# Kernel tuning notes

Measured on AMD Instinct MI355X. Metric: run time of the kernel, lower is better.

## Reference

```python
import jax, jax.numpy as jnp
import numpy as np

DIM = 512
CTX = 768
GROUPS = 32
EPS = 1e-5


def setup_inputs() -> dict:
    key = jax.random.key(0)
    ks = jax.random.split(key, 12)
    B, H, W, S = 16, 64, 64, 256
    x = jax.random.normal(ks[0], (B, DIM, H, W), dtype=jnp.float32)
    context = jax.random.normal(ks[1], (B, S, CTX), dtype=jnp.float32)
    gn_w = jnp.ones((DIM,), jnp.float32)
    gn_b = jnp.zeros((DIM,), jnp.float32)
    ln_w = jnp.ones((CTX,), jnp.float32)
    ln_b = jnp.zeros((CTX,), jnp.float32)
    wq = jax.random.normal(ks[2], (DIM, DIM), jnp.float32) * (DIM ** -0.5)
    bq = jnp.zeros((DIM,), jnp.float32)
    wkv = jax.random.normal(ks[3], (2 * DIM, CTX), jnp.float32) * (CTX ** -0.5)
    bkv = jnp.zeros((2 * DIM,), jnp.float32)
    wo = jax.random.normal(ks[4], (DIM, DIM), jnp.float32) * (DIM ** -0.5)
    bo = jnp.zeros((DIM,), jnp.float32)
    return {"x": x, "context": context, "gn_w": gn_w, "gn_b": gn_b,
            "ln_w": ln_w, "ln_b": ln_b, "wq": wq, "bq": bq,
            "wkv": wkv, "bkv": bkv, "wo": wo, "bo": bo}


def reference(x, context, gn_w, gn_b, ln_w, ln_b, wq, bq, wkv, bkv, wo, bo):
    b, c, h, w = x.shape
    scale = c ** -0.5
    # GroupNorm over (channels-per-group, H, W)
    xr = x.reshape(b, GROUPS, -1)
    mu = xr.mean(-1, keepdims=True)
    var = xr.var(-1, keepdims=True)
    xn = ((xr - mu) * jax.lax.rsqrt(var + EPS)).reshape(b, c, h, w)
    xn = xn * gn_w[None, :, None, None] + gn_b[None, :, None, None]
    # 1x1 conv query projection as channel GEMM
    q = jnp.einsum('bchw,oc->bohw', xn, wq) + bq[None, :, None, None]
    q = q.reshape(b, c, h * w).transpose(0, 2, 1)  # b, hw, c
    # LayerNorm on context
    cm = context.mean(-1, keepdims=True)
    cv = context.var(-1, keepdims=True)
    cn = (context - cm) * jax.lax.rsqrt(cv + EPS) * ln_w + ln_b
    kv = cn @ wkv.T + bkv  # b, s, 2c
    k, v = jnp.split(kv, 2, axis=-1)
    sim = jnp.einsum('bic,bjc->bij', q, k) * scale
    attn = jax.nn.softmax(sim, axis=-1)
    out = jnp.einsum('bij,bjc->bic', attn, v)
    out = out.transpose(0, 2, 1).reshape(b, c, h, w)
    out = jnp.einsum('bchw,oc->bohw', out, wo) + bo[None, :, None, None]
    return out + x
```

## Files before the change

### kernel.cpp

```cpp
#include <hip/hip_runtime.h>

typedef unsigned short u16;
typedef __attribute__((ext_vector_type(8))) short short8;
typedef __attribute__((ext_vector_type(4))) float f32x4;

#define DIM 512
#define CTX 768
#define HW 4096
#define NB 16
#define NS 256
#define EPSV 1e-5f

__device__ inline u16 f2bf(float f) {
    union { float f; unsigned u; } x; x.f = f;
    unsigned r = x.u + 0x7fffu + ((x.u >> 16) & 1u);
    return (u16)(r >> 16);
}
__device__ inline float bf2f(u16 v) {
    union { unsigned u; float f; } x; x.u = (unsigned)v << 16; return x.f;
}

__global__ void gn_stats(const float* __restrict__ x, const float* __restrict__ gn_w,
                         const float* __restrict__ gn_b, float* __restrict__ ga,
                         float* __restrict__ gd) {
    const int bg = blockIdx.x;
    const int b = bg >> 5, g = bg & 31;
    const float* base = x + ((long)b * DIM + g * 16) * HW;
    float s1 = 0.f, s2 = 0.f;
    const int tid = threadIdx.x;
    for (int i = tid; i < 16384; i += 256) {
        float4 v = ((const float4*)base)[i];
        s1 += v.x + v.y + v.z + v.w;
        s2 += v.x * v.x + v.y * v.y + v.z * v.z + v.w * v.w;
    }
    __shared__ float r1[256], r2[256];
    r1[tid] = s1; r2[tid] = s2; __syncthreads();
    for (int s = 128; s > 0; s >>= 1) {
        if (tid < s) { r1[tid] += r1[tid + s]; r2[tid] += r2[tid + s]; }
        __syncthreads();
    }
    __shared__ float mu_s, rs_s;
    if (tid == 0) {
        float mu = r1[0] * (1.f / 65536.f);
        float var = r2[0] * (1.f / 65536.f) - mu * mu;
        mu_s = mu; rs_s = rsqrtf(var + EPSV);
    }
    __syncthreads();
    if (tid < 16) {
        int c = g * 16 + tid;
        float aa = rs_s * gn_w[c];
        ga[b * DIM + c] = aa;
        gd[b * DIM + c] = gn_b[c] - mu_s * aa;
    }
}

__global__ void gn_apply_t(const float* __restrict__ x, const float* __restrict__ ga,
                           const float* __restrict__ gd, u16* __restrict__ xnt) {
    const int b = blockIdx.y;
    const int c0 = (blockIdx.x & 7) * 64;
    const int p0 = (blockIdx.x >> 3) * 64;
    __shared__ u16 t[64][68];
    const int tid = threadIdx.x;
    const int tc = tid >> 4;
    const int tp = (tid & 15) * 4;
    #pragma unroll
    for (int i = 0; i < 4; i++) {
        const int c = c0 + tc + i * 16;
        const float a = ga[b * DIM + c];
        const float d = gd[b * DIM + c];
        float4 v = *(const float4*)&x[((long)b * DIM + c) * HW + p0 + tp];
        u16* dst = &t[tc + i * 16][tp];
        dst[0] = f2bf(v.x * a + d);
        dst[1] = f2bf(v.y * a + d);
        dst[2] = f2bf(v.z * a + d);
        dst[3] = f2bf(v.w * a + d);
    }
    __syncthreads();
    const int wp = tid >> 3;
    const int wc = (tid & 7) * 8;
    #pragma unroll
    for (int i = 0; i < 2; i++) {
        const int p = wp + i * 32;
        short8 o;
        #pragma unroll
        for (int k = 0; k < 8; k++) o[k] = t[wc + k][p];
        *(short8*)&xnt[((long)b * HW + p0 + p) * DIM + c0 + wc] = o;
    }
}

__global__ void ln_ctx(const float* __restrict__ ctx, const float* __restrict__ ln_w,
                       const float* __restrict__ ln_b, u16* __restrict__ cn) {
    const int row = blockIdx.x;
    const int tid = threadIdx.x;
    const float* r = ctx + (long)row * CTX;
    float v[3]; float s1 = 0.f, s2 = 0.f;
    #pragma unroll
    for (int i = 0; i < 3; i++) { v[i] = r[tid + i * 256]; s1 += v[i]; s2 += v[i] * v[i]; }
    __shared__ float r1[256], r2[256];
    r1[tid] = s1; r2[tid] = s2; __syncthreads();
    for (int s = 128; s > 0; s >>= 1) {
        if (tid < s) { r1[tid] += r1[tid + s]; r2[tid] += r2[tid + s]; }
        __syncthreads();
    }
    __shared__ float mu_s, rs_s;
    if (tid == 0) {
        float mu = r1[0] * (1.f / 768.f);
        float var = r2[0] * (1.f / 768.f) - mu * mu;
        mu_s = mu; rs_s = rsqrtf(var + EPSV);
    }
    __syncthreads();
    #pragma unroll
    for (int i = 0; i < 3; i++) {
        int idx = tid + i * 256;
        cn[(long)row * CTX + idx] = f2bf((v[i] - mu_s) * rs_s * ln_w[idx] + ln_b[idx]);
    }
}

__global__ void cvt_weights(const float* __restrict__ wq, const float* __restrict__ wkv,
                            const float* __restrict__ wo, u16* __restrict__ wqtb,
                            u16* __restrict__ wkvb, u16* __restrict__ wob) {
    int i = blockIdx.x * 256 + threadIdx.x;
    if (i < 262144) {
        wqtb[(i & 511) * 512 + (i >> 9)] = f2bf(wq[i]);
        wob[i] = f2bf(wo[i]);
    }
    if (i < 786432) wkvb[i] = f2bf(wkv[i]);
}

__global__ void kbias_k(const u16* __restrict__ k, const float* __restrict__ bq,
                        float* __restrict__ kbias) {
    const int row = blockIdx.x;
    const int tid = threadIdx.x;
    const u16* r = k + (long)row * DIM;
    float s = bf2f(r[tid]) * bq[tid] + bf2f(r[tid + 256]) * bq[tid + 256];
    __shared__ float red[256];
    red[tid] = s; __syncthreads();
    for (int st = 128; st > 0; st >>= 1) {
        if (tid < st) red[tid] += red[tid + st];
        __syncthreads();
    }
    if (tid == 0) kbias[row] = red[0];
}

template <int EPI>
__launch_bounds__(256, 2)
__global__ void gemm_nt(const u16* __restrict__ A, const u16* __restrict__ Bm,
                        const float* __restrict__ bias,
                        void* __restrict__ out0, void* __restrict__ out1,
                        int M, int N, int K, long batchA, long batchB,
                        long obatch, int ldo) {
    __shared__ u16 As[128][56];
    __shared__ u16 Bs[128][56];
    const int tid = threadIdx.x;
    const int lane = tid & 63;
    const int wave = tid >> 6;
    const int bb = blockIdx.y;
    const int tiles_n = N >> 7;
    const int m0 = (blockIdx.x / tiles_n) << 7;
    const int n0 = (blockIdx.x % tiles_n) << 7;
    const u16* Ab = A + (long)bb * batchA + (long)m0 * K;
    const u16* Bb = Bm + (long)bb * batchB + (long)n0 * K;

    const int sr = tid >> 2;
    const int sc = (tid & 3) << 3;
    const int l16 = lane & 15;
    const int quad = lane >> 4;
    const int wr = (wave >> 1) << 6;
    const int wc = (wave & 1) << 6;

    f32x4 acc[4][4] = {};

    for (int k0 = 0; k0 < K; k0 += 32) {
        __syncthreads();
        *(short8*)&As[sr][sc]      = *(const short8*)(Ab + (long)sr * K + k0 + sc);
        *(short8*)&As[sr + 64][sc] = *(const short8*)(Ab + (long)(sr + 64) * K + k0 + sc);
        *(short8*)&Bs[sr][sc]      = *(const short8*)(Bb + (long)sr * K + k0 + sc);
        *(short8*)&Bs[sr + 64][sc] = *(const short8*)(Bb + (long)(sr + 64) * K + k0 + sc);
        __syncthreads();
        short8 af[4], bfr[4];
        #pragma unroll
        for (int i = 0; i < 4; i++) af[i] = *(const short8*)&As[wr + i * 16 + l16][quad * 8];
        #pragma unroll
        for (int j = 0; j < 4; j++) bfr[j] = *(const short8*)&Bs[wc + j * 16 + l16][quad * 8];
        #pragma unroll
        for (int i = 0; i < 4; i++)
            #pragma unroll
            for (int j = 0; j < 4; j++)
                acc[i][j] = __builtin_amdgcn_mfma_f32_16x16x32_bf16(af[i], bfr[j], acc[i][j], 0, 0, 0);
    }

    #pragma unroll
    for (int i = 0; i < 4; i++) {
        #pragma unroll
        for (int r = 0; r < 4; r++) {
            const int row = m0 + wr + i * 16 + quad * 4 + r;
            #pragma unroll
            for (int j = 0; j < 4; j++) {
                const int col = n0 + wc + j * 16 + l16;
                float v = acc[i][j][r];
                if (EPI == 0) {
                    v += bias[col];
                    if (col < DIM) ((u16*)out0)[(long)bb * obatch + (long)row * ldo + col] = f2bf(v);
                    else           ((u16*)out1)[(long)bb * obatch + (long)row * ldo + (col - DIM)] = f2bf(v);
                } else if (EPI == 3) {
                    ((u16*)out0)[(long)bb * obatch + (long)row * ldo + col] = f2bf(v);
                } else {
                    ((u16*)out0)[(long)bb * obatch + (long)col * ldo + row] = f2bf(v);
                }
            }
        }
    }
}

__launch_bounds__(512, 4)
__global__ void flash_attn(const u16* __restrict__ xnt, const u16* __restrict__ Kq,
                           const u16* __restrict__ Vot, const float* __restrict__ kbias,
                           const float* __restrict__ bo, const float* __restrict__ x,
                           float* __restrict__ out) {
    __shared__ __align__(16) char fsm[78080];
    u16 (*As)[56]      = (u16(*)[56])(fsm);
    u16 (*Bs)[56]      = (u16(*)[56])(fsm + 14336);
    u16 (*P)[264]      = (u16(*)[264])(fsm);
    float (*red)[4]    = (float(*)[4])(fsm + 67584);
    float (*lbuf)[132] = (float(*)[132])(fsm + 69632);

    const int tid = threadIdx.x;
    const int lane = tid & 63;
    const int wave = tid >> 6;
    const int mw = wave >> 2;
    const int nw = wave & 3;
    const int l16 = lane & 15;
    const int quad = lane >> 4;
    const int b = blockIdx.y;
    const int m0 = blockIdx.x << 7;

    const u16* Ab = xnt + ((long)b * HW + m0) * DIM;
    const u16* Bb = Kq + (long)b * NS * DIM;

    f32x4 acc[4][4] = {};
    for (int k0 = 0; k0 < DIM; k0 += 32) {
        __syncthreads();
        {
            const int r = tid >> 2, c = (tid & 3) << 3;
            *(short8*)&As[r][c] = *(const short8*)(Ab + (long)r * DIM + k0 + c);
            const int r2 = tid >> 1, c2 = (tid & 1) << 4;
            *(short8*)&Bs[r2][c2]     = *(const short8*)(Bb + (long)r2 * DIM + k0 + c2);
            *(short8*)&Bs[r2][c2 + 8] = *(const short8*)(Bb + (long)r2 * DIM + k0 + c2 + 8);
        }
        __syncthreads();
        short8 af[4], bfr[4];
        #pragma unroll
        for (int i = 0; i < 4; i++) af[i] = *(const short8*)&As[mw * 64 + i * 16 + l16][quad * 8];
        #pragma unroll
        for (int j = 0; j < 4; j++) bfr[j] = *(const short8*)&Bs[nw * 64 + j * 16 + l16][quad * 8];
        #pragma unroll
        for (int i = 0; i < 4; i++)
            #pragma unroll
            for (int j = 0; j < 4; j++)
                acc[i][j] = __builtin_amdgcn_mfma_f32_16x16x32_bf16(af[i], bfr[j], acc[i][j], 0, 0, 0);
    }

    const float scale = 0.044194173824159216f;
    float kb[4];
    #pragma unroll
    for (int j = 0; j < 4; j++) kb[j] = kbias[b * NS + nw * 64 + j * 16 + l16];

    #pragma unroll
    for (int i = 0; i < 4; i++) {
        #pragma unroll
        for (int r = 0; r < 4; r++) {
            float m = -1e30f;
            #pragma unroll
            for (int j = 0; j < 4; j++) {
                float v = (acc[i][j][r] + kb[j]) * scale;
                acc[i][j][r] = v;
                m = fmaxf(m, v);
            }
            #pragma unroll
            for (int off = 1; off < 16; off <<= 1) m = fmaxf(m, __shfl_xor(m, off));
            if (l16 == 0) red[mw * 64 + i * 16 + quad * 4 + r][nw] = m;
        }
    }
    __syncthreads();
    float rsum[4][4];
    #pragma unroll
    for (int i = 0; i < 4; i++) {
        #pragma unroll
        for (int r = 0; r < 4; r++) {
            const int row = mw * 64 + i * 16 + quad * 4 + r;
            float4 rv = *(const float4*)red[row];
            float gm = fmaxf(fmaxf(rv.x, rv.y), fmaxf(rv.z, rv.w));
            float s = 0.f;
            #pragma unroll
            for (int j = 0; j < 4; j++) {
                float e = __expf(acc[i][j][r] - gm);
                acc[i][j][r] = e;
                s += e;
            }
            #pragma unroll
            for (int off = 1; off < 16; off <<= 1) s += __shfl_xor(s, off);
            rsum[i][r] = s;
        }
    }
    __syncthreads();
    #pragma unroll
    for (int i = 0; i < 4; i++)
        #pragma unroll
        for (int r = 0; r < 4; r++)
            if (l16 == 0) red[mw * 64 + i * 16 + quad * 4 + r][nw] = rsum[i][r];
    __syncthreads();
    #pragma unroll
    for (int i = 0; i < 4; i++) {
        #pragma unroll
        for (int r = 0; r < 4; r++) {
            const int row = mw * 64 + i * 16 + quad * 4 + r;
            float4 sv = *(const float4*)red[row];
            float inv = 1.f / (sv.x + sv.y + sv.z + sv.w);
            #pragma unroll
            for (int j = 0; j < 4; j++)
                P[row][nw * 64 + j * 16 + l16] = f2bf(acc[i][j][r] * inv);
        }
    }
    __syncthreads();

    const u16* Vb = Vot + ((long)b * DIM + nw * 32 + l16) * NS + quad * 8;
    for (int nc = 0; nc < 4; nc++) {
        f32x4 oacc[4][2];
        #pragma unroll
        for (int i = 0; i < 4; i++)
            #pragma unroll
            for (int jj = 0; jj < 2; jj++)
                oacc[i][jj] = (f32x4){0.f, 0.f, 0.f, 0.f};
        #pragma unroll
        for (int kk = 0; kk < 8; kk++) {
            short8 pf[4], vf[2];
            #pragma unroll
            for (int i = 0; i < 4; i++)
                pf[i] = *(const short8*)&P[mw * 64 + i * 16 + l16][kk * 32 + quad * 8];
            #pragma unroll
            for (int jj = 0; jj < 2; jj++)
                vf[jj] = *(const short8*)(Vb + (long)(nc * 128 + jj * 16) * NS + kk * 32);
            #pragma unroll
            for (int i = 0; i < 4; i++)
                #pragma unroll
                for (int jj = 0; jj < 2; jj++)
                    oacc[i][jj] = __builtin_amdgcn_mfma_f32_16x16x32_bf16(pf[i], vf[jj], oacc[i][jj], 0, 0, 0);
        }
        #pragma unroll
        for (int t = 0; t < 8; t++) {
            __syncthreads();
            if (nw == (t >> 1)) {
                const int jj = t & 1;
                #pragma unroll
                for (int i = 0; i < 4; i++)
                    #pragma unroll
                    for (int r = 0; r < 4; r++)
                        lbuf[l16][mw * 64 + i * 16 + quad * 4 + r] = oacc[i][jj][r];
            }
            __syncthreads();
            {
                const int cl = tid >> 5;
                const int p4 = (tid & 31) * 4;
                const int cg = nc * 128 + t * 16 + cl;
                const long idx = ((long)b * DIM + cg) * HW + m0 + p4;
                const float bv = bo[cg];
                float4 v0 = *(const float4*)&lbuf[cl][p4];
                float4 x0 = *(const float4*)&x[idx];
                v0.x += x0.x + bv; v0.y += x0.y + bv; v0.z += x0.z + bv; v0.w += x0.w + bv;
                *(float4*)&out[idx] = v0;
            }
        }
    }
}

extern "C" void kernel_launch(void* const* d_in, const int* in_sizes, int n_in,
                              void* d_out, int out_size, void* d_ws, size_t ws_size,
                              hipStream_t stream) {
    const float* x    = (const float*)d_in[0];
    const float* ctx  = (const float*)d_in[1];
    const float* gn_w = (const float*)d_in[2];
    const float* gn_b = (const float*)d_in[3];
    const float* ln_w = (const float*)d_in[4];
    const float* ln_b = (const float*)d_in[5];
    const float* wq   = (const float*)d_in[6];
    const float* bq   = (const float*)d_in[7];
    const float* wkv  = (const float*)d_in[8];
    const float* bkv  = (const float*)d_in[9];
    const float* wo   = (const float*)d_in[10];
    const float* bo   = (const float*)d_in[11];

    char* ws = (char*)d_ws;
    u16*   xnt  = (u16*)(ws + 0);
    u16*   cn   = (u16*)(ws + 67108864);
    u16*   kb_  = (u16*)(ws + 73400320);
    u16*   vb_  = (u16*)(ws + 77594624);
    u16*   Kq   = (u16*)(ws + 81788928);
    u16*   Vot  = (u16*)(ws + 85983232);
    u16*   wqtb = (u16*)(ws + 90177536);
    u16*   wkvb = (u16*)(ws + 90701824);
    u16*   wob  = (u16*)(ws + 92274688);
    float* ga   = (float*)(ws + 92798976);
    float* gd   = ga + NB * DIM;
    float* kbias = (float*)(ws + 92864512);

    gn_stats<<<dim3(NB * 32), dim3(256), 0, stream>>>(x, gn_w, gn_b, ga, gd);
    gn_apply_t<<<dim3(512, NB), dim3(256), 0, stream>>>(x, ga, gd, xnt);
    ln_ctx<<<dim3(NB * NS), dim3(256), 0, stream>>>(ctx, ln_w, ln_b, cn);
    cvt_weights<<<dim3(3072), dim3(256), 0, stream>>>(wq, wkv, wo, wqtb, wkvb, wob);

    gemm_nt<0><<<dim3(2 * 8, NB), dim3(256), 0, stream>>>(
        cn, wkvb, bkv, kb_, vb_, NS, 2 * DIM, CTX,
        (long)NS * CTX, 0, (long)NS * DIM, DIM);
    gemm_nt<3><<<dim3(2 * 4, NB), dim3(256), 0, stream>>>(
        kb_, wqtb, nullptr, Kq, nullptr, NS, DIM, DIM,
        (long)NS * DIM, 0, (long)NS * DIM, DIM);
    kbias_k<<<dim3(NB * NS), dim3(256), 0, stream>>>(kb_, bq, kbias);
    gemm_nt<5><<<dim3(2 * 4, NB), dim3(256), 0, stream>>>(
        vb_, wob, nullptr, Vot, nullptr, NS, DIM, DIM,
        (long)NS * DIM, 0, (long)DIM * NS, NS);
    flash_attn<<<dim3(32, NB), dim3(512), 0, stream>>>(
        xnt, Kq, Vot, kbias, bo, x, (float*)d_out);
}
```

Before: 441.9 us.

## Register-prefetch GEMM tiles, merge Q/V projection launches, write attention output directly

In the GEMMs and the flash attention QK loop, the next K-slice is loaded into registers while MFMAs run on the current shared-memory tile, which overlaps global-load latency with compute. The two small projection GEMMs (K·Wq and V·Wo) are merged into one launch using blockIdx.z, removing a launch and filling more CUs. The attention epilogue no longer stages through shared memory with 16 barriers; each lane writes float4 results plus bias and residual straight to global memory. The cost is higher register pressure and possibly less coalesced stores in the epilogue.

```diff
diff --git a/kernel.cpp b/kernel.cpp
--- a/kernel.cpp
+++ b/kernel.cpp
@@ -142,24 +142,20 @@
     if (tid == 0) kbias[row] = red[0];
 }
 
-template <int EPI>
 __launch_bounds__(256, 2)
-__global__ void gemm_nt(const u16* __restrict__ A, const u16* __restrict__ Bm,
+__global__ void gemm_kv(const u16* __restrict__ A, const u16* __restrict__ Bm,
                         const float* __restrict__ bias,
-                        void* __restrict__ out0, void* __restrict__ out1,
-                        int M, int N, int K, long batchA, long batchB,
-                        long obatch, int ldo) {
+                        u16* __restrict__ outk, u16* __restrict__ outv) {
     __shared__ u16 As[128][56];
     __shared__ u16 Bs[128][56];
     const int tid = threadIdx.x;
     const int lane = tid & 63;
     const int wave = tid >> 6;
     const int bb = blockIdx.y;
-    const int tiles_n = N >> 7;
-    const int m0 = (blockIdx.x / tiles_n) << 7;
-    const int n0 = (blockIdx.x % tiles_n) << 7;
-    const u16* Ab = A + (long)bb * batchA + (long)m0 * K;
-    const u16* Bb = Bm + (long)bb * batchB + (long)n0 * K;
+    const int m0 = (blockIdx.x >> 3) << 7;
+    const int n0 = (blockIdx.x & 7) << 7;
+    const u16* Ab = A + (long)bb * NS * CTX + (long)m0 * CTX;
+    const u16* Bb = Bm + (long)n0 * CTX;
 
     const int sr = tid >> 2;
     const int sc = (tid & 3) << 3;
@@ -168,15 +164,29 @@
     const int wr = (wave >> 1) << 6;
     const int wc = (wave & 1) << 6;
 
+    const u16* Ap0 = Ab + (long)sr * CTX + sc;
+    const u16* Ap1 = Ab + (long)(sr + 64) * CTX + sc;
+    const u16* Bp0 = Bb + (long)sr * CTX + sc;
+    const u16* Bp1 = Bb + (long)(sr + 64) * CTX + sc;
+    short8 rA0 = *(const short8*)Ap0;
+    short8 rA1 = *(const short8*)Ap1;
+    short8 rB0 = *(const short8*)Bp0;
+    short8 rB1 = *(const short8*)Bp1;
+
     f32x4 acc[4][4] = {};
-
-    for (int k0 = 0; k0 < K; k0 += 32) {
-        __syncthreads();
-        *(short8*)&As[sr][sc]      = *(const short8*)(Ab + (long)sr * K + k0 + sc);
-        *(short8*)&As[sr + 64][sc] = *(const short8*)(Ab + (long)(sr + 64) * K + k0 + sc);
-        *(short8*)&Bs[sr][sc]      = *(const short8*)(Bb + (long)sr * K + k0 + sc);
-        *(short8*)&Bs[sr + 64][sc] = *(const short8*)(Bb + (long)(sr + 64) * K + k0 + sc);
-        __syncthreads();
+    for (int k0 = 0; k0 < CTX; k0 += 32) {
+        if (k0) __syncthreads();
+        *(short8*)&As[sr][sc]      = rA0;
+        *(short8*)&As[sr + 64][sc] = rA1;
+        *(short8*)&Bs[sr][sc]      = rB0;
+        *(short8*)&Bs[sr + 64][sc] = rB1;
+        __syncthreads();
+        if (k0 + 32 < CTX) {
+            rA0 = *(const short8*)(Ap0 + k0 + 32);
+            rA1 = *(const short8*)(Ap1 + k0 + 32);
+            rB0 = *(const short8*)(Bp0 + k0 + 32);
+            rB1 = *(const short8*)(Bp1 + k0 + 32);
+        }
         short8 af[4], bfr[4];
         #pragma unroll
         for (int i = 0; i < 4; i++) af[i] = *(const short8*)&As[wr + i * 16 + l16][quad * 8];
@@ -197,16 +207,83 @@
             #pragma unroll
             for (int j = 0; j < 4; j++) {
                 const int col = n0 + wc + j * 16 + l16;
-                float v = acc[i][j][r];
-                if (EPI == 0) {
-                    v += bias[col];
-                    if (col < DIM) ((u16*)out0)[(long)bb * obatch + (long)row * ldo + col] = f2bf(v);
-                    else           ((u16*)out1)[(long)bb * obatch + (long)row * ldo + (col - DIM)] = f2bf(v);
-                } else if (EPI == 3) {
-                    ((u16*)out0)[(long)bb * obatch + (long)row * ldo + col] = f2bf(v);
-                } else {
-                    ((u16*)out0)[(long)bb * obatch + (long)col * ldo + row] = f2bf(v);
-                }
+                float v = acc[i][j][r] + bias[col];
+                if (col < DIM) outk[(long)bb * NS * DIM + (long)row * DIM + col] = f2bf(v);
+                else           outv[(long)bb * NS * DIM + (long)row * DIM + (col - DIM)] = f2bf(v);
+            }
+        }
+    }
+}
+
+__launch_bounds__(256, 2)
+__global__ void gemm_qv(const u16* __restrict__ kb_, const u16* __restrict__ vb_,
+                        const u16* __restrict__ wqtb, const u16* __restrict__ wob,
+                        u16* __restrict__ Kq, u16* __restrict__ Vot) {
+    __shared__ u16 As[128][56];
+    __shared__ u16 Bs[128][56];
+    const int tid = threadIdx.x;
+    const int lane = tid & 63;
+    const int wave = tid >> 6;
+    const int bb = blockIdx.y;
+    const bool isV = blockIdx.z != 0;
+    const int m0 = (blockIdx.x >> 2) << 7;
+    const int n0 = (blockIdx.x & 3) << 7;
+    const u16* Ab = (isV ? vb_ : kb_) + (long)bb * NS * DIM + (long)m0 * DIM;
+    const u16* Bb = (isV ? wob : wqtb) + (long)n0 * DIM;
+
+    const int sr = tid >> 2;
+    const int sc = (tid & 3) << 3;
+    const int l16 = lane & 15;
+    const int quad = lane >> 4;
+    const int wr = (wave >> 1) << 6;
+    const int wc = (wave & 1) << 6;
+
+    const u16* Ap0 = Ab + (long)sr * DIM + sc;
+    const u16* Ap1 = Ab + (long)(sr + 64) * DIM + sc;
+    const u16* Bp0 = Bb + (long)sr * DIM + sc;
+    const u16* Bp1 = Bb + (long)(sr + 64) * DIM + sc;
+    short8 rA0 = *(const short8*)Ap0;
+    short8 rA1 = *(const short8*)Ap1;
+    short8 rB0 = *(const short8*)Bp0;
+    short8 rB1 = *(const short8*)Bp1;
+
+    f32x4 acc[4][4] = {};
+    for (int k0 = 0; k0 < DIM; k0 += 32) {
+        if (k0) __syncthreads();
+        *(short8*)&As[sr][sc]      = rA0;
+        *(short8*)&As[sr + 64][sc] = rA1;
+        *(short8*)&Bs[sr][sc]      = rB0;
+        *(short8*)&Bs[sr + 64][sc] = rB1;
+        __syncthreads();
+        if (k0 + 32 < DIM) {
+            rA0 = *(const short8*)(Ap0 + k0 + 32);
+            rA1 = *(const short8*)(Ap1 + k0 + 32);
+            rB0 = *(const short8*)(Bp0 + k0 + 32);
+            rB1 = *(const short8*)(Bp1 + k0 + 32);
+        }
+        short8 af[4], bfr[4];
+        #pragma unroll
+        for (int i = 0; i < 4; i++) af[i] = *(const short8*)&As[wr + i * 16 + l16][quad * 8];
+        #pragma unroll
+        for (int j = 0; j < 4; j++) bfr[j] = *(const short8*)&Bs[wc + j * 16 + l16][quad * 8];
+        #pragma unroll
+        for (int i = 0; i < 4; i++)
+            #pragma unroll
+            for (int j = 0; j < 4; j++)
+                acc[i][j] = __builtin_amdgcn_mfma_f32_16x16x32_bf16(af[i], bfr[j], acc[i][j], 0, 0, 0);
+    }
+
+    #pragma unroll
+    for (int i = 0; i < 4; i++) {
+        #pragma unroll
+        for (int r = 0; r < 4; r++) {
+            const int row = m0 + wr + i * 16 + quad * 4 + r;
+            #pragma unroll
+            for (int j = 0; j < 4; j++) {
+                const int col = n0 + wc + j * 16 + l16;
+                const u16 v = f2bf(acc[i][j][r]);
+                if (!isV) Kq[(long)bb * NS * DIM + (long)row * DIM + col] = v;
+                else      Vot[(long)bb * DIM * NS + (long)col * NS + row] = v;
             }
         }
     }
@@ -217,12 +294,11 @@
                            const u16* __restrict__ Vot, const float* __restrict__ kbias,
                            const float* __restrict__ bo, const float* __restrict__ x,
                            float* __restrict__ out) {
-    __shared__ __align__(16) char fsm[78080];
+    __shared__ __align__(16) char fsm[69632];
     u16 (*As)[56]      = (u16(*)[56])(fsm);
     u16 (*Bs)[56]      = (u16(*)[56])(fsm + 14336);
     u16 (*P)[264]      = (u16(*)[264])(fsm);
     float (*red)[4]    = (float(*)[4])(fsm + 67584);
-    float (*lbuf)[132] = (float(*)[132])(fsm + 69632);
 
     const int tid = threadIdx.x;
     const int lane = tid & 63;
@@ -237,17 +313,26 @@
     const u16* Ab = xnt + ((long)b * HW + m0) * DIM;
     const u16* Bb = Kq + (long)b * NS * DIM;
 
+    const int rS = tid >> 2, cS = (tid & 3) << 3;
+    const int rB = tid >> 1, cB = (tid & 1) << 4;
+    const u16* Ap = Ab + (long)rS * DIM + cS;
+    const u16* Bp = Bb + (long)rB * DIM + cB;
+    short8 rA  = *(const short8*)(Ap);
+    short8 rB0 = *(const short8*)(Bp);
+    short8 rB1 = *(const short8*)(Bp + 8);
+
     f32x4 acc[4][4] = {};
     for (int k0 = 0; k0 < DIM; k0 += 32) {
-        __syncthreads();
-        {
-            const int r = tid >> 2, c = (tid & 3) << 3;
-            *(short8*)&As[r][c] = *(const short8*)(Ab + (long)r * DIM + k0 + c);
-            const int r2 = tid >> 1, c2 = (tid & 1) << 4;
-            *(short8*)&Bs[r2][c2]     = *(const short8*)(Bb + (long)r2 * DIM + k0 + c2);
-            *(short8*)&Bs[r2][c2 + 8] = *(const short8*)(Bb + (long)r2 * DIM + k0 + c2 + 8);
-        }
-        __syncthreads();
+        if (k0) __syncthreads();
+        *(short8*)&As[rS][cS]     = rA;
+        *(short8*)&Bs[rB][cB]     = rB0;
+        *(short8*)&Bs[rB][cB + 8] = rB1;
+        __syncthreads();
+        if (k0 + 32 < DIM) {
+            rA  = *(const short8*)(Ap + k0 + 32);
+            rB0 = *(const short8*)(Bp + k0 + 32);
+            rB1 = *(const short8*)(Bp + k0 + 40);
+        }
         short8 af[4], bfr[4];
         #pragma unroll
         for (int i = 0; i < 4; i++) af[i] = *(const short8*)&As[mw * 64 + i * 16 + l16][quad * 8];
@@ -347,27 +432,19 @@
                     oacc[i][jj] = __builtin_amdgcn_mfma_f32_16x16x32_bf16(pf[i], vf[jj], oacc[i][jj], 0, 0, 0);
         }
         #pragma unroll
-        for (int t = 0; t < 8; t++) {
-            __syncthreads();
-            if (nw == (t >> 1)) {
-                const int jj = t & 1;
-                #pragma unroll
-                for (int i = 0; i < 4; i++)
-                    #pragma unroll
-                    for (int r = 0; r < 4; r++)
-                        lbuf[l16][mw * 64 + i * 16 + quad * 4 + r] = oacc[i][jj][r];
-            }
-            __syncthreads();
-            {
-                const int cl = tid >> 5;
-                const int p4 = (tid & 31) * 4;
-                const int cg = nc * 128 + t * 16 + cl;
-                const long idx = ((long)b * DIM + cg) * HW + m0 + p4;
-                const float bv = bo[cg];
-                float4 v0 = *(const float4*)&lbuf[cl][p4];
-                float4 x0 = *(const float4*)&x[idx];
-                v0.x += x0.x + bv; v0.y += x0.y + bv; v0.z += x0.z + bv; v0.w += x0.w + bv;
-                *(float4*)&out[idx] = v0;
+        for (int jj = 0; jj < 2; jj++) {
+            const int c = nc * 128 + nw * 32 + jj * 16 + l16;
+            const float bv = bo[c];
+            const long base = ((long)b * DIM + c) * HW + m0 + mw * 64 + quad * 4;
+            #pragma unroll
+            for (int i = 0; i < 4; i++) {
+                float4 xv = *(const float4*)&x[base + i * 16];
+                float4 o;
+                o.x = oacc[i][jj][0] + xv.x + bv;
+                o.y = oacc[i][jj][1] + xv.y + bv;
+                o.z = oacc[i][jj][2] + xv.z + bv;
+                o.w = oacc[i][jj][3] + xv.w + bv;
+                *(float4*)&out[base + i * 16] = o;
             }
         }
     }
@@ -408,16 +485,9 @@
     ln_ctx<<<dim3(NB * NS), dim3(256), 0, stream>>>(ctx, ln_w, ln_b, cn);
     cvt_weights<<<dim3(3072), dim3(256), 0, stream>>>(wq, wkv, wo, wqtb, wkvb, wob);
 
-    gemm_nt<0><<<dim3(2 * 8, NB), dim3(256), 0, stream>>>(
-        cn, wkvb, bkv, kb_, vb_, NS, 2 * DIM, CTX,
-        (long)NS * CTX, 0, (long)NS * DIM, DIM);
-    gemm_nt<3><<<dim3(2 * 4, NB), dim3(256), 0, stream>>>(
-        kb_, wqtb, nullptr, Kq, nullptr, NS, DIM, DIM,
-        (long)NS * DIM, 0, (long)NS * DIM, DIM);
+    gemm_kv<<<dim3(2 * 8, NB), dim3(256), 0, stream>>>(cn, wkvb, bkv, kb_, vb_);
+    gemm_qv<<<dim3(2 * 4, NB, 2), dim3(256), 0, stream>>>(kb_, vb_, wqtb, wob, Kq, Vot);
     kbias_k<<<dim3(NB * NS), dim3(256), 0, stream>>>(kb_, bq, kbias);
-    gemm_nt<5><<<dim3(2 * 4, NB), dim3(256), 0, stream>>>(
-        vb_, wob, nullptr, Vot, nullptr, NS, DIM, DIM,
-        (long)NS * DIM, 0, (long)DIM * NS, NS);
     flash_attn<<<dim3(32, NB), dim3(512), 0, stream>>>(
         xnt, Kq, Vot, kbias, bo, x, (float*)d_out);
 }
```

Result: no change. 450.7 us (+2.0%).
